# Performance work log

Measured on AMD Instinct MI355X. Metric: run time of the kernel, lower is better.

## Reference

```python
import jax, jax.numpy as jnp
import numpy as np


def setup_inputs() -> dict:
    key = jax.random.key(0)
    k1, k2, k3, k4, k5 = jax.random.split(key, 5)
    B, H, W, C, F = 8, 64, 64, 256, 64
    # glorot_uniform for 1x1 conv kernels [1,1,Cin,Cout]
    def glorot(k, cin, cout):
        lim = float(np.sqrt(6.0 / (cin + cout)))
        return jax.random.uniform(k, (1, 1, cin, cout), jnp.float32, -lim, lim)
    x = jax.random.normal(k1, (B, H, W, C), dtype=jnp.float32)
    Wf = glorot(k2, C, F)
    Wg = glorot(k3, C, F)
    Wh = glorot(k4, C, C)
    Wv = glorot(k5, C, C)
    gamma = jnp.zeros((1,), dtype=jnp.float32) + 0.1  # nonzero so attention path matters
    return {"x": x, "Wf": Wf, "Wg": Wg, "Wh": Wh, "Wv": Wv, "gamma": gamma}


def reference(x, Wf, Wg, Wh, Wv, gamma):
    B, H, W, C = x.shape
    N = H * W
    # 1x1 convs are pointwise matmuls over channels
    f = jnp.einsum('bhwc,cf->bhwf', x, Wf[0, 0])   # [B,H,W,F]
    g = jnp.einsum('bhwc,cf->bhwf', x, Wg[0, 0])   # [B,H,W,F]
    h = jnp.einsum('bhwc,cd->bhwd', x, Wh[0, 0])   # [B,H,W,C]
    ff = f.reshape(B, N, -1)                        # [B,N,F]
    gf = g.reshape(B, N, -1)                        # [B,N,F]
    hf = h.reshape(B, N, C)                         # [B,N,C]
    # s[b,i,j] = ff[b,i,:] . gf[b,j,:]  (no 1/sqrt(d) scaling, as in source)
    s = jnp.einsum('bif,bjf->bij', ff, gf)          # [B,N,N]
    beta = jax.nn.softmax(s, axis=-1)
    o = jnp.einsum('bij,bjc->bic', beta, hf)        # [B,N,C]
    o = o.reshape(B, H, W, C)
    o = jnp.einsum('bhwc,cd->bhwd', o, Wv[0, 0])
    return gamma * o + x
```

## Files before the change

### kernel.cpp

```cpp
#include <hip/hip_runtime.h>

typedef _Float16 half8   __attribute__((ext_vector_type(8)));
typedef _Float16 half4_t __attribute__((ext_vector_type(4)));
typedef float    float4_t __attribute__((ext_vector_type(4)));

#define B_   8
#define N_   4096
#define C_   256
#define F_   64

#if defined(__has_builtin) && __has_builtin(__builtin_amdgcn_exp2f)
#define EXP2(x) __builtin_amdgcn_exp2f(x)
#else
#define EXP2(x) exp2f(x)
#endif
#define LOG2E 1.44269504f

static __device__ __forceinline__ float4_t mfma16(half8 a, half8 b, float4_t c) {
  return __builtin_amdgcn_mfma_f32_16x16x32_f16(a, b, c, 0, 0, 0);
}

template <int CTRL>
static __device__ __forceinline__ float dpp_f(float x) {
  return __int_as_float(__builtin_amdgcn_update_dpp(
      __float_as_int(x), __float_as_int(x), CTRL, 0xF, 0xF, false));
}
static __device__ __forceinline__ float row_max16(float v) {
  v = fmaxf(v, dpp_f<0x128>(v));
  v = fmaxf(v, dpp_f<0x124>(v));
  v = fmaxf(v, dpp_f<0x122>(v));
  v = fmaxf(v, dpp_f<0x121>(v));
  return v;
}
static __device__ __forceinline__ float row_sum16(float v) {
  v += dpp_f<0x128>(v);
  v += dpp_f<0x124>(v);
  v += dpp_f<0x122>(v);
  v += dpp_f<0x121>(v);
  return v;
}

__global__ __launch_bounds__(256) void prep_kernel(const float* __restrict__ Wh,
                                                   const float* __restrict__ Wv,
                                                   const float* __restrict__ Wf,
                                                   const float* __restrict__ Wg,
                                                   _Float16* __restrict__ whvt,
                                                   _Float16* __restrict__ wfgt) {
  int c = threadIdx.x;
  if (blockIdx.x < 256) {
    int d = blockIdx.x;
    const float4_t* whr = (const float4_t*)(Wh + (size_t)c * 256);
    float acc = 0.f;
#pragma unroll 8
    for (int e4 = 0; e4 < 64; ++e4) {
      float4_t w4 = whr[e4];
      acc += w4[0] * Wv[(e4 * 4 + 0) * 256 + d];
      acc += w4[1] * Wv[(e4 * 4 + 1) * 256 + d];
      acc += w4[2] * Wv[(e4 * 4 + 2) * 256 + d];
      acc += w4[3] * Wv[(e4 * 4 + 3) * 256 + d];
    }
    whvt[d * 256 + c] = (_Float16)acc;
  } else {
    int n = blockIdx.x - 256;
    float v = (n < 64) ? Wf[c * 64 + n] * LOG2E : Wg[c * 64 + (n - 64)];
    wfgt[n * 256 + c] = (_Float16)v;
  }
}

__global__ __launch_bounds__(256) void fgt_kernel(const float* __restrict__ x,
                                                  const _Float16* __restrict__ wfgt,
                                                  _Float16* __restrict__ f,
                                                  _Float16* __restrict__ g,
                                                  _Float16* __restrict__ xT) {
  __shared__ float tile[2][32][33];
  int tid  = threadIdx.x;
  int wave = tid >> 6, lane = tid & 63;
  int n16  = lane & 15, quad = lane >> 4;
  const int wrow = wave & 1;
  const int wcol = wave >> 1;
  int row  = blockIdx.x * 32 + wrow * 16 + n16;
  float4_t acc[4];
#pragma unroll
  for (int t = 0; t < 4; t++) acc[t] = (float4_t){0.f, 0.f, 0.f, 0.f};
  for (int k0 = 0; k0 < 256; k0 += 32) {
    const float* xp = x + (size_t)row * C_ + k0 + quad * 8;
    float4_t x0 = *(const float4_t*)xp;
    float4_t x1 = *(const float4_t*)(xp + 4);
    half8 af;
#pragma unroll
    for (int j = 0; j < 4; j++) { af[j] = (_Float16)x0[j]; af[4 + j] = (_Float16)x1[j]; }
#pragma unroll
    for (int t = 0; t < 4; t++) {
      half8 bf = *(const half8*)(wfgt +
                  (size_t)(wcol * 64 + t * 16 + n16) * 256 + k0 + quad * 8);
      acc[t] = mfma16(af, bf, acc[t]);
    }
  }
  int orow = blockIdx.x * 32 + wrow * 16 + quad * 4;
  _Float16* dstfg = wcol ? g : f;
#pragma unroll
  for (int t = 0; t < 4; t++) {
#pragma unroll
    for (int r = 0; r < 4; r++) {
      dstfg[(size_t)(orow + r) * 64 + t * 16 + n16] = (_Float16)acc[t][r];
    }
  }

  const int b   = blockIdx.x >> 7;
  const int nb  = (blockIdx.x & 127) << 5;
  const int tr  = tid >> 3;
  const int tc  = (tid & 7) << 2;
#pragma unroll 1
  for (int s = 0; s < 4; ++s) {
    const int c0p = s << 6;
    __syncthreads();
#pragma unroll
    for (int h = 0; h < 2; ++h) {
      const float* src = x + ((size_t)(b * N_ + nb + tr)) * C_ + c0p + h * 32 + tc;
      float4_t v = *(const float4_t*)src;
      tile[h][tr][tc + 0] = v[0]; tile[h][tr][tc + 1] = v[1];
      tile[h][tr][tc + 2] = v[2]; tile[h][tr][tc + 3] = v[3];
    }
    __syncthreads();
#pragma unroll
    for (int h = 0; h < 2; ++h) {
      half4_t o;
      o[0] = (_Float16)tile[h][tc + 0][tr];
      o[1] = (_Float16)tile[h][tc + 1][tr];
      o[2] = (_Float16)tile[h][tc + 2][tr];
      o[3] = (_Float16)tile[h][tc + 3][tr];
      _Float16* dst = xT + ((size_t)(b * C_ + c0p + h * 32 + tr)) * N_ + nb + tc;
      *(half4_t*)dst = o;
    }
  }
}

__global__ __launch_bounds__(256, 2) void flash_kernel(const _Float16* __restrict__ f,
                                                       const _Float16* __restrict__ g,
                                                       const _Float16* __restrict__ xT,
                                                       _Float16* __restrict__ a) {
  __shared__ _Float16 ktb2[2][64 * 64];
  __shared__ _Float16 ptb2[2][64 * 64];
  __shared__ float alpha_lds[2][64];
  __shared__ float linv_lds[64];

  const int b   = blockIdx.x;
  const int i0  = blockIdx.y * 64;
  const int tid = threadIdx.x;
  const int wave = tid >> 6, lane = tid & 63;
  const int n16 = lane & 15, quad = lane >> 4;
  const int nlo = n16 & 7, nhi = n16 >> 3;

  half8 qf[2];
  {
    const _Float16* qp = f + (size_t)(b * N_ + i0 + wave * 16 + n16) * 64 + quad * 8;
    qf[0] = *(const half8*)qp;
    qf[1] = *(const half8*)(qp + 32);
  }

  float4_t o_acc[16];
#pragma unroll
  for (int t = 0; t < 16; t++) o_acc[t] = (float4_t){0.f, 0.f, 0.f, 0.f};
  float m_i[4] = {-1e30f, -1e30f, -1e30f, -1e30f};
  float l_i[4] = {0.f, 0.f, 0.f, 0.f};

  const _Float16* gbase = g + (size_t)(b * N_) * 64;
  const _Float16* xbase = xT + ((size_t)b * C_ + 64 * wave) * (size_t)N_;

  const int krow = tid >> 2;
  const int kcb  = (tid & 3) << 1;
  const int krb  = krow & 7;

  {
    const _Float16* ks = gbase + (size_t)krow * 64 + (kcb << 3);
    half8 k0 = *(const half8*)ks;
    half8 k1 = *(const half8*)(ks + 8);
    _Float16* kd = ktb2[0] + krow * 64;
    *(half8*)(kd + (((kcb    ) ^ krb) << 3)) = k0;
    *(half8*)(kd + (((kcb + 1) ^ krb) << 3)) = k1;
  }
  __syncthreads();

  for (int k = 0; k < 64; ++k) {
    const int j0  = k << 6;
    const int buf = k & 1;
    const int j0n = (j0 + 64) & (N_ - 1);

    half8 kp0, kp1;
    {
      const _Float16* ks = gbase + (size_t)(j0n + krow) * 64 + (kcb << 3);
      kp0 = *(const half8*)ks;
      kp1 = *(const half8*)(ks + 8);
    }
    half8 vfr[8];
#pragma unroll
    for (int s = 0; s < 2; s++)
#pragma unroll
      for (int ct = 0; ct < 4; ct++)
        vfr[s * 4 + ct] = *(const half8*)(xbase + (size_t)(16 * ct + n16) * N_ +
                                          j0 + 32 * s + 8 * quad);

    float4_t s_acc[4];
#pragma unroll
    for (int t = 0; t < 4; t++) s_acc[t] = (float4_t){0.f, 0.f, 0.f, 0.f};
    {
      const _Float16* ktb = ktb2[buf];
      __builtin_amdgcn_s_setprio(1);
#pragma unroll
      for (int s = 0; s < 2; s++)
#pragma unroll
        for (int t = 0; t < 4; t++) {
          half8 bf = *(const half8*)(ktb + (16 * t + n16) * 64 +
                                     (((4 * s + quad) ^ nlo) << 3));
          s_acc[t] = mfma16(qf[s], bf, s_acc[t]);
        }
      __builtin_amdgcn_s_setprio(0);
    }

    float alpha_r[4];
#pragma unroll
    for (int r = 0; r < 4; r++) {
      float v = fmaxf(fmaxf(s_acc[0][r], s_acc[1][r]),
                      fmaxf(s_acc[2][r], s_acc[3][r]));
      v = row_max16(v);
      float mn = fmaxf(m_i[r], v);
      alpha_r[r] = EXP2(m_i[r] - mn);
      m_i[r] = mn;
    }
    _Float16* pb = ptb2[buf];
#pragma unroll
    for (int r = 0; r < 4; r++) {
      float s0 = EXP2(s_acc[0][r] - m_i[r]);
      float s1 = EXP2(s_acc[1][r] - m_i[r]);
      float s2 = EXP2(s_acc[2][r] - m_i[r]);
      float s3 = EXP2(s_acc[3][r] - m_i[r]);
      float v = row_sum16(s0 + s1 + s2 + s3);
      l_i[r] = l_i[r] * alpha_r[r] + v;
      const int row = wave * 16 + 4 * quad + r;
      const int rb  = row & 7;
      _Float16* pr = pb + row * 64 + nlo;
      pr[((nhi    ) ^ rb) << 3] = (_Float16)s0;
      pr[((nhi + 2) ^ rb) << 3] = (_Float16)s1;
      pr[((nhi + 4) ^ rb) << 3] = (_Float16)s2;
      pr[((nhi + 6) ^ rb) << 3] = (_Float16)s3;
    }
    if (n16 == 0) {
#pragma unroll
      for (int r = 0; r < 4; r++)
        alpha_lds[buf][wave * 16 + 4 * quad + r] = alpha_r[r];
    }
    {
      _Float16* kd = ktb2[buf ^ 1] + krow * 64;
      *(half8*)(kd + (((kcb    ) ^ krb) << 3)) = kp0;
      *(half8*)(kd + (((kcb + 1) ^ krb) << 3)) = kp1;
    }
    __syncthreads();

#pragma unroll
    for (int ti = 0; ti < 4; ti++)
#pragma unroll
      for (int r = 0; r < 4; r++) {
        float al = alpha_lds[buf][ti * 16 + 4 * quad + r];
#pragma unroll
        for (int ct = 0; ct < 4; ct++) o_acc[ti * 4 + ct][r] *= al;
      }

    __builtin_amdgcn_s_setprio(1);
#pragma unroll
    for (int s = 0; s < 2; s++)
#pragma unroll
      for (int ti = 0; ti < 4; ti++) {
        half8 af = *(const half8*)(pb + (16 * ti + n16) * 64 +
                                   (((4 * s + quad) ^ nlo) << 3));
#pragma unroll
        for (int ct = 0; ct < 4; ct++)
          o_acc[ti * 4 + ct] = mfma16(af, vfr[s * 4 + ct], o_acc[ti * 4 + ct]);
      }
    __builtin_amdgcn_s_setprio(0);
  }

  if (n16 == 0) {
#pragma unroll
    for (int r = 0; r < 4; r++)
      linv_lds[wave * 16 + 4 * quad + r] = 1.f / l_i[r];
  }
  __syncthreads();
#pragma unroll
  for (int ti = 0; ti < 4; ti++)
#pragma unroll
    for (int r = 0; r < 4; r++) {
      float il = linv_lds[ti * 16 + 4 * quad + r];
      size_t orow = (size_t)(b * N_ + i0 + ti * 16 + 4 * quad + r) * C_;
#pragma unroll
      for (int ct = 0; ct < 4; ct++)
        a[orow + 64 * wave + 16 * ct + n16] =
            (_Float16)(o_acc[ti * 4 + ct][r] * il);
    }
}

__global__ __launch_bounds__(256) void out_kernel(const _Float16* __restrict__ a,
                                                  const _Float16* __restrict__ whvt,
                                                  const float* __restrict__ x,
                                                  const float* __restrict__ gamma,
                                                  float* __restrict__ out) {
  int tid  = threadIdx.x;
  int wave = tid >> 6, lane = tid & 63;
  int n16  = lane & 15, quad = lane >> 4;
  int row  = blockIdx.x * 64 + wave * 16 + n16;
  int col0 = blockIdx.y * 64;
  float4_t acc[4];
#pragma unroll
  for (int t = 0; t < 4; t++) acc[t] = (float4_t){0.f, 0.f, 0.f, 0.f};
  for (int k0 = 0; k0 < 256; k0 += 32) {
    half8 af = *(const half8*)(a + (size_t)row * C_ + k0 + quad * 8);
#pragma unroll
    for (int t = 0; t < 4; t++) {
      half8 bf = *(const half8*)(whvt +
                  (size_t)(col0 + t * 16 + n16) * 256 + k0 + quad * 8);
      acc[t] = mfma16(af, bf, acc[t]);
    }
  }
  float gm = gamma[0];
  int orow = blockIdx.x * 64 + wave * 16 + quad * 4;
#pragma unroll
  for (int t = 0; t < 4; t++) {
#pragma unroll
    for (int r = 0; r < 4; r++) {
      size_t idx = (size_t)(orow + r) * C_ + col0 + t * 16 + n16;
      out[idx] = gm * acc[t][r] + x[idx];
    }
  }
}

extern "C" void kernel_launch(void* const* d_in, const int* in_sizes, int n_in,
                              void* d_out, int out_size, void* d_ws, size_t ws_size,
                              hipStream_t stream) {
  const float* x     = (const float*)d_in[0];
  const float* Wf    = (const float*)d_in[1];
  const float* Wg    = (const float*)d_in[2];
  const float* Wh    = (const float*)d_in[3];
  const float* Wv    = (const float*)d_in[4];
  const float* gamma = (const float*)d_in[5];
  float* out = (float*)d_out;

  char* w = (char*)d_ws;
  _Float16* whvt = (_Float16*)(w);
  _Float16* wfgt = (_Float16*)(w + 131072);
  _Float16* fb   = (_Float16*)(w + 196608);
  _Float16* gb   = (_Float16*)(w + 196608 + 4194304);
  _Float16* xT   = (_Float16*)(w + 196608 + 2 * 4194304);
  _Float16* ab   = (_Float16*)(w + 196608 + 2 * 4194304 + 16777216);

  hipLaunchKernelGGL(prep_kernel, dim3(384),    dim3(256), 0, stream,
                     Wh, Wv, Wf, Wg, whvt, wfgt);
  hipLaunchKernelGGL(fgt_kernel,  dim3(1024),   dim3(256), 0, stream,
                     x, wfgt, fb, gb, xT);
  hipLaunchKernelGGL(flash_kernel, dim3(8, 64), dim3(256), 0, stream, fb, gb, xT, ab);
  hipLaunchKernelGGL(out_kernel,  dim3(512, 4), dim3(256), 0, stream,
                     ab, whvt, x, gamma, out);
}
```

Before: 285.9 us.

## Fuse output projection and residual epilogue into flash attention kernel

The normalized attention output tile is staged into shared memory, reusing the K/P buffers, then multiplied by the combined Wh·Wv weights inside the flash kernel, which adds gamma-scaled residual x and writes the final output. This removes the separate out_kernel launch and the fp16 intermediate buffer round-trip through global memory. In exchange it adds an extra epilogue to each flash block and raises register pressure (16 more accumulators) in a kernel limited to two blocks per CU. Each block now also reads the full 256x256 weight matrix from global memory.

```diff
diff --git a/kernel.cpp b/kernel.cpp
--- a/kernel.cpp
+++ b/kernel.cpp
@@ -138,9 +138,11 @@
 __global__ __launch_bounds__(256, 2) void flash_kernel(const _Float16* __restrict__ f,
                                                        const _Float16* __restrict__ g,
                                                        const _Float16* __restrict__ xT,
-                                                       _Float16* __restrict__ a) {
-  __shared__ _Float16 ktb2[2][64 * 64];
-  __shared__ _Float16 ptb2[2][64 * 64];
+                                                       const _Float16* __restrict__ whvt,
+                                                       const float* __restrict__ x,
+                                                       const float* __restrict__ gamma,
+                                                       float* __restrict__ out) {
+  __shared__ _Float16 smem[16896];
   __shared__ float alpha_lds[2][64];
   __shared__ float linv_lds[64];
 
@@ -175,7 +177,7 @@
     const _Float16* ks = gbase + (size_t)krow * 64 + (kcb << 3);
     half8 k0 = *(const half8*)ks;
     half8 k1 = *(const half8*)(ks + 8);
-    _Float16* kd = ktb2[0] + krow * 64;
+    _Float16* kd = smem + krow * 64;
     *(half8*)(kd + (((kcb    ) ^ krb) << 3)) = k0;
     *(half8*)(kd + (((kcb + 1) ^ krb) << 3)) = k1;
   }
@@ -204,7 +206,7 @@
 #pragma unroll
     for (int t = 0; t < 4; t++) s_acc[t] = (float4_t){0.f, 0.f, 0.f, 0.f};
     {
-      const _Float16* ktb = ktb2[buf];
+      const _Float16* ktb = smem + buf * 4096;
       __builtin_amdgcn_s_setprio(1);
 #pragma unroll
       for (int s = 0; s < 2; s++)
@@ -227,7 +229,7 @@
       alpha_r[r] = EXP2(m_i[r] - mn);
       m_i[r] = mn;
     }
-    _Float16* pb = ptb2[buf];
+    _Float16* pb = smem + 8192 + buf * 4096;
 #pragma unroll
     for (int r = 0; r < 4; r++) {
       float s0 = EXP2(s_acc[0][r] - m_i[r]);
@@ -250,7 +252,7 @@
         alpha_lds[buf][wave * 16 + 4 * quad + r] = alpha_r[r];
     }
     {
-      _Float16* kd = ktb2[buf ^ 1] + krow * 64;
+      _Float16* kd = smem + (buf ^ 1) * 4096 + krow * 64;
       *(half8*)(kd + (((kcb    ) ^ krb) << 3)) = kp0;
       *(half8*)(kd + (((kcb + 1) ^ krb) << 3)) = kp1;
     }
@@ -285,51 +287,57 @@
       linv_lds[wave * 16 + 4 * quad + r] = 1.f / l_i[r];
   }
   __syncthreads();
+  __builtin_amdgcn_sched_barrier(0);
+
 #pragma unroll
   for (int ti = 0; ti < 4; ti++)
 #pragma unroll
     for (int r = 0; r < 4; r++) {
-      float il = linv_lds[ti * 16 + 4 * quad + r];
-      size_t orow = (size_t)(b * N_ + i0 + ti * 16 + 4 * quad + r) * C_;
-#pragma unroll
-      for (int ct = 0; ct < 4; ct++)
-        a[orow + 64 * wave + 16 * ct + n16] =
+      const int row = ti * 16 + 4 * quad + r;
+      const int rb  = row & 7;
+      float il = linv_lds[row];
+#pragma unroll
+      for (int ct = 0; ct < 4; ct++) {
+        const int cb = (wave << 3) + (ct << 1) + nhi;
+        smem[row * 256 + ((cb ^ rb) << 3) + nlo] =
             (_Float16)(o_acc[ti * 4 + ct][r] * il);
-    }
-}
-
-__global__ __launch_bounds__(256) void out_kernel(const _Float16* __restrict__ a,
-                                                  const _Float16* __restrict__ whvt,
-                                                  const float* __restrict__ x,
-                                                  const float* __restrict__ gamma,
-                                                  float* __restrict__ out) {
-  int tid  = threadIdx.x;
-  int wave = tid >> 6, lane = tid & 63;
-  int n16  = lane & 15, quad = lane >> 4;
-  int row  = blockIdx.x * 64 + wave * 16 + n16;
-  int col0 = blockIdx.y * 64;
-  float4_t acc[4];
-#pragma unroll
-  for (int t = 0; t < 4; t++) acc[t] = (float4_t){0.f, 0.f, 0.f, 0.f};
+      }
+    }
+  __syncthreads();
+  __builtin_amdgcn_sched_barrier(0);
+
+  float4_t ep[16];
+#pragma unroll
+  for (int t = 0; t < 16; t++) ep[t] = (float4_t){0.f, 0.f, 0.f, 0.f};
   for (int k0 = 0; k0 < 256; k0 += 32) {
-    half8 af = *(const half8*)(a + (size_t)row * C_ + k0 + quad * 8);
-#pragma unroll
-    for (int t = 0; t < 4; t++) {
+    half8 af[4];
+#pragma unroll
+    for (int mi = 0; mi < 4; mi++) {
+      const int row = mi * 16 + n16;
+      const int kb  = ((k0 >> 3) + quad) ^ (row & 7);
+      af[mi] = *(const half8*)(smem + row * 256 + (kb << 3));
+    }
+#pragma unroll
+    for (int ct = 0; ct < 4; ct++) {
       half8 bf = *(const half8*)(whvt +
-                  (size_t)(col0 + t * 16 + n16) * 256 + k0 + quad * 8);
-      acc[t] = mfma16(af, bf, acc[t]);
-    }
-  }
-  float gm = gamma[0];
-  int orow = blockIdx.x * 64 + wave * 16 + quad * 4;
-#pragma unroll
-  for (int t = 0; t < 4; t++) {
-#pragma unroll
-    for (int r = 0; r < 4; r++) {
-      size_t idx = (size_t)(orow + r) * C_ + col0 + t * 16 + n16;
-      out[idx] = gm * acc[t][r] + x[idx];
-    }
-  }
+                  (size_t)(wave * 64 + ct * 16 + n16) * 256 + k0 + quad * 8);
+#pragma unroll
+      for (int mi = 0; mi < 4; mi++)
+        ep[mi * 4 + ct] = mfma16(af[mi], bf, ep[mi * 4 + ct]);
+    }
+  }
+  const float gm = gamma[0];
+#pragma unroll
+  for (int mi = 0; mi < 4; mi++)
+#pragma unroll
+    for (int r = 0; r < 4; r++) {
+      size_t orow = (size_t)(b * N_ + i0 + mi * 16 + 4 * quad + r) * C_;
+#pragma unroll
+      for (int ct = 0; ct < 4; ct++) {
+        size_t idx = orow + wave * 64 + ct * 16 + n16;
+        out[idx] = gm * ep[mi * 4 + ct][r] + x[idx];
+      }
+    }
 }
 
 extern "C" void kernel_launch(void* const* d_in, const int* in_sizes, int n_in,
@@ -349,13 +357,11 @@
   _Float16* fb   = (_Float16*)(w + 196608);
   _Float16* gb   = (_Float16*)(w + 196608 + 4194304);
   _Float16* xT   = (_Float16*)(w + 196608 + 2 * 4194304);
-  _Float16* ab   = (_Float16*)(w + 196608 + 2 * 4194304 + 16777216);
 
   hipLaunchKernelGGL(prep_kernel, dim3(384),    dim3(256), 0, stream,
                      Wh, Wv, Wf, Wg, whvt, wfgt);
   hipLaunchKernelGGL(fgt_kernel,  dim3(1024),   dim3(256), 0, stream,
                      x, wfgt, fb, gb, xT);
-  hipLaunchKernelGGL(flash_kernel, dim3(8, 64), dim3(256), 0, stream, fb, gb, xT, ab);
-  hipLaunchKernelGGL(out_kernel,  dim3(512, 4), dim3(256), 0, stream,
-                     ab, whvt, x, gamma, out);
-}
+  hipLaunchKernelGGL(flash_kernel, dim3(8, 64), dim3(256), 0, stream,
+                     fb, gb, xT, whvt, x, gamma, out);
+}
```

Measured after the change: 259.5 us. 9.2% less time.
